# Kernel tuning notes

Measured on AMD Instinct MI355X. Metric: run time of the kernel, lower is better.

## Reference

```python
import jax, jax.numpy as jnp
import numpy as np


def setup_inputs() -> dict:
    key = jax.random.key(0)
    ks = jax.random.split(key, 5)
    b, t, q_dim, kv_dim, h = 16, 128, 256, 64, 4
    c = t - 1
    q_x = jax.random.normal(ks[0], (b, t, q_dim), dtype=jnp.float32)
    kv_x = jax.random.normal(ks[1], (b, t, c, kv_dim), dtype=jnp.float32)
    # Linear weights stored as [in, out]; no biases (bias=False in torch module).
    sq = 1.0 / np.sqrt(q_dim)
    sk = 1.0 / np.sqrt(kv_dim)
    Wq = jax.random.uniform(ks[2], (q_dim, kv_dim * h), jnp.float32, -sq, sq)
    Wk = jax.random.uniform(ks[3], (kv_dim, kv_dim * h), jnp.float32, -sk, sk)
    Wv = jax.random.uniform(ks[4], (kv_dim, kv_dim * h), jnp.float32, -sk, sk)
    return {"q_x": q_x, "kv_x": kv_x, "Wq": Wq, "Wk": Wk, "Wv": Wv}


def reference(q_x, kv_x, Wq, Wk, Wv):
    b, t, c, k = kv_x.shape  # c = t - 1
    h = Wq.shape[1] // k
    # projections
    q = (q_x @ Wq).reshape(b, t, h, k)          # [b,t,h,k]
    keys = (kv_x @ Wk).reshape(b, t, c, h, k)   # [b,t,c,h,k]
    vals = (kv_x @ Wv).reshape(b, t, c, h, k)
    # per-token attention over the c-sized context
    scores = jnp.einsum('bthk,btchk->bthc', q, keys) / jnp.sqrt(jnp.float32(k))
    w = jax.nn.softmax(scores, axis=-1)          # softmax over context dim
    out = jnp.einsum('bthc,btchk->bthk', w, vals)
    return out.reshape(b, t, h * k)
```

## Files before the change

kernel.cpp:

```cpp
#include <hip/hip_runtime.h>
#include <math.h>

#define Bdim 16
#define Tdim 128
#define Cdim 127
#define Hdim 4
#define QD   256
#define HK   256
#define BT   (Bdim * Tdim)

#define DPP_XOR1        0xB1
#define DPP_XOR2        0x4E
#define DPP_HALF_MIRROR 0x141
#define DPP_MIRROR      0x140
template<int CTRL>
__device__ __forceinline__ float dpp_movf(float x) {
    return __int_as_float(__builtin_amdgcn_update_dpp(
        0, __float_as_int(x), CTRL, 0xF, 0xF, true));
}
__device__ __forceinline__ float quad_sum(float v) {
    v += dpp_movf<DPP_XOR1>(v);
    v += dpp_movf<DPP_XOR2>(v);
    return v;
}
__device__ __forceinline__ float rows_max(float v) {
    v = fmaxf(v, dpp_movf<DPP_HALF_MIRROR>(v));
    v = fmaxf(v, dpp_movf<DPP_MIRROR>(v));
    v = fmaxf(v, __shfl_xor(v, 16, 64));
    v = fmaxf(v, __shfl_xor(v, 32, 64));
    return v;
}
__device__ __forceinline__ float rows_sum(float v) {
    v += dpp_movf<DPP_HALF_MIRROR>(v);
    v += dpp_movf<DPP_MIRROR>(v);
    v += __shfl_xor(v, 16, 64);
    v += __shfl_xor(v, 32, 64);
    return v;
}
__device__ __forceinline__ float wx_red(float v) {
    v += dpp_movf<DPP_XOR1>(v);
    v += dpp_movf<DPP_XOR2>(v);
    v += dpp_movf<DPP_HALF_MIRROR>(v);
    v += dpp_movf<DPP_MIRROR>(v);
    v += __shfl_xor(v, 16, 64);
    return v;
}

__global__ __launch_bounds__(256) void precompute_M(
        const float* __restrict__ Wq, const float* __restrict__ Wk,
        float* __restrict__ M) {
    __shared__ float wk_s[64][129];
    __shared__ float wq_s[2][128];
    int I = blockIdx.x;
    int H = blockIdx.y;
    int tid = threadIdx.x;

    #pragma unroll
    for (int it = 0; it < 8; ++it) {
        int flat = tid + it * 256;
        int m = flat >> 5, kq = flat & 31;
        float4 v = *(const float4*)(Wk + m * HK + H * 128 + kq * 4);
        wk_s[m][kq*4+0] = v.x; wk_s[m][kq*4+1] = v.y;
        wk_s[m][kq*4+2] = v.z; wk_s[m][kq*4+3] = v.w;
    }
    if (tid < 64) {
        int r = tid >> 5, kq = tid & 31;
        float4 v = *(const float4*)(Wq + (size_t)(I*2+r) * HK + H * 128 + kq * 4);
        wq_s[r][kq*4+0] = v.x; wq_s[r][kq*4+1] = v.y;
        wq_s[r][kq*4+2] = v.z; wq_s[r][kq*4+3] = v.w;
    }
    __syncthreads();

    int r = tid >> 7, hh = (tid >> 6) & 1, m = tid & 63;
    float acc = 0.f;
    #pragma unroll 8
    for (int j = 0; j < 64; ++j)
        acc = fmaf(wq_s[r][hh*64+j], wk_s[m][hh*64+j], acc);
    M[(size_t)(I*2+r) * HK + H * 128 + hh * 64 + m] = acc;
}

template <int NS>
__global__ __launch_bounds__(256) void qk_gemm(
        const float* __restrict__ q_x,
        const float* __restrict__ M,
        float* __restrict__ part) {
    const int KLEN = 256 / NS;
    __shared__ __align__(16) float q_s[16][256 / NS];
    int RB = blockIdx.x;
    int S  = blockIdx.y;
    int tid = threadIdx.x;

    for (int f = tid; f < 16 * KLEN / 4; f += 256) {
        int r = f / (KLEN / 4), kq = f % (KLEN / 4);
        *(float4*)&q_s[r][kq*4] =
            *(const float4*)(q_x + (size_t)(RB*16 + r) * QD + S * KLEN + kq * 4);
    }
    __syncthreads();

    float acc[16];
    #pragma unroll
    for (int r = 0; r < 16; ++r) acc[r] = 0.f;

    for (int kk = 0; kk < KLEN / 4; ++kk) {
        int k = S * KLEN + kk * 4;
        float m0 = M[(size_t)(k+0) * HK + tid];
        float m1 = M[(size_t)(k+1) * HK + tid];
        float m2 = M[(size_t)(k+2) * HK + tid];
        float m3 = M[(size_t)(k+3) * HK + tid];
        #pragma unroll
        for (int r = 0; r < 16; ++r) {
            float4 qv = *(const float4*)&q_s[r][kk*4];
            acc[r] = fmaf(qv.x, m0, fmaf(qv.y, m1, fmaf(qv.z, m2, fmaf(qv.w, m3, acc[r]))));
        }
    }
    float* dst = part + (size_t)S * (BT*HK) + (size_t)RB * 16 * HK + tid;
    #pragma unroll
    for (int r = 0; r < 16; ++r) dst[r * HK] = acc[r];
}

template <int NS>
__global__ __launch_bounds__(512, 6) void attn_main(
        const float* __restrict__ kv_x,
        const float* __restrict__ qk_p,
        const float* __restrict__ Wv,
        float* __restrict__ out) {
    __shared__ __align__(16) float4 sX4[128 * 16];
    __shared__ __align__(16) float qk_s[HK];
    __shared__ __align__(16) float4 e4[128];
    __shared__ __align__(16) float4 wx4[Hdim * 16];
    __shared__ __align__(16) float4 redm[8];
    __shared__ __align__(16) float4 reds[8];

    int bt  = blockIdx.x;
    int tid = threadIdx.x;

    const float4* Xg = (const float4*)(kv_x + (size_t)bt * (Cdim * 64));
    #pragma unroll
    for (int it = 0; it < 4; ++it) {
        int l = tid + it * 512;
        if (l < Cdim * 16) {
            int c = l >> 4, p = l & 15;
            __builtin_amdgcn_global_load_lds(
                (const __attribute__((address_space(1))) void*)(Xg + (c << 4) + (p ^ (c & 7))),
                (__attribute__((address_space(3))) void*)(sX4 + l), 16, 0, 0);
        }
    }
    if (tid >= 256 && tid < 320)
        ((float*)sX4)[Cdim * 64 + (tid - 256)] = 0.f;
    if (tid < 256) {
        float q = 0.f;
        #pragma unroll
        for (int s = 0; s < NS; ++s)
            q += qk_p[(size_t)s * (BT*HK) + (size_t)bt * HK + tid];
        qk_s[tid] = q;
    }
    __syncthreads();

    int lane = tid & 63;
    int wave = tid >> 6;
    int c  = tid >> 2;
    int qp = tid & 3;
    int sw = c & 7;

    float s0, s1, s2, s3;
    {
        const float4* xrow = sX4 + c * 16;
        float4 x0 = xrow[(qp*4 + 0) ^ sw];
        float4 x1 = xrow[(qp*4 + 1) ^ sw];
        float4 x2 = xrow[(qp*4 + 2) ^ sw];
        float4 x3 = xrow[(qp*4 + 3) ^ sw];
        const float4* qk4 = (const float4*)qk_s;
        float a0 = 0.f, a1 = 0.f, a2 = 0.f, a3 = 0.f;
        #pragma unroll
        for (int i = 0; i < 4; ++i) {
            float4 xi = (i == 0) ? x0 : (i == 1) ? x1 : (i == 2) ? x2 : x3;
            float4 q0 = qk4[0*16 + qp*4 + i];
            float4 q1 = qk4[1*16 + qp*4 + i];
            float4 q2 = qk4[2*16 + qp*4 + i];
            float4 q3 = qk4[3*16 + qp*4 + i];
            a0 = fmaf(q0.x, xi.x, fmaf(q0.y, xi.y, fmaf(q0.z, xi.z, fmaf(q0.w, xi.w, a0))));
            a1 = fmaf(q1.x, xi.x, fmaf(q1.y, xi.y, fmaf(q1.z, xi.z, fmaf(q1.w, xi.w, a1))));
            a2 = fmaf(q2.x, xi.x, fmaf(q2.y, xi.y, fmaf(q2.z, xi.z, fmaf(q2.w, xi.w, a2))));
            a3 = fmaf(q3.x, xi.x, fmaf(q3.y, xi.y, fmaf(q3.z, xi.z, fmaf(q3.w, xi.w, a3))));
        }
        a0 = quad_sum(a0); a1 = quad_sum(a1); a2 = quad_sum(a2); a3 = quad_sum(a3);
        bool valid = (c < Cdim);
        s0 = valid ? a0 * 0.125f : -INFINITY;
        s1 = valid ? a1 * 0.125f : -INFINITY;
        s2 = valid ? a2 * 0.125f : -INFINITY;
        s3 = valid ? a3 * 0.125f : -INFINITY;
    }

    float m0 = rows_max(s0), m1 = rows_max(s1), m2 = rows_max(s2), m3 = rows_max(s3);
    if (lane == 0) redm[wave] = make_float4(m0, m1, m2, m3);
    __syncthreads();
    float4 gm = redm[0];
    #pragma unroll
    for (int w = 1; w < 8; ++w) {
        float4 r = redm[w];
        gm.x = fmaxf(gm.x, r.x); gm.y = fmaxf(gm.y, r.y);
        gm.z = fmaxf(gm.z, r.z); gm.w = fmaxf(gm.w, r.w);
    }
    float e0 = __expf(s0 - gm.x);
    float e1 = __expf(s1 - gm.y);
    float e2 = __expf(s2 - gm.z);
    float e3 = __expf(s3 - gm.w);
    if (qp == 0) e4[c] = make_float4(e0, e1, e2, e3);
    float t0 = rows_sum(e0), t1 = rows_sum(e1), t2 = rows_sum(e2), t3 = rows_sum(e3);
    if (lane == 0) reds[wave] = make_float4(t0, t1, t2, t3);
    __syncthreads();

    {
        int jc = tid >> 5;
        int mq = (lane >> 3) & 3;
        int cs = lane & 7;
        float4 A0 = {0,0,0,0}, A1 = {0,0,0,0}, A2 = {0,0,0,0}, A3 = {0,0,0,0};
        #pragma unroll
        for (int mm = 0; mm < 4; ++mm) {
            int cc = cs + 8 * (mq * 4 + mm);
            float4 x4 = sX4[cc * 16 + (jc ^ cs)];
            float4 ee = e4[cc];
            A0.x = fmaf(ee.x, x4.x, A0.x); A0.y = fmaf(ee.x, x4.y, A0.y);
            A0.z = fmaf(ee.x, x4.z, A0.z); A0.w = fmaf(ee.x, x4.w, A0.w);
            A1.x = fmaf(ee.y, x4.x, A1.x); A1.y = fmaf(ee.y, x4.y, A1.y);
            A1.z = fmaf(ee.y, x4.z, A1.z); A1.w = fmaf(ee.y, x4.w, A1.w);
            A2.x = fmaf(ee.z, x4.x, A2.x); A2.y = fmaf(ee.z, x4.y, A2.y);
            A2.z = fmaf(ee.z, x4.z, A2.z); A2.w = fmaf(ee.z, x4.w, A2.w);
            A3.x = fmaf(ee.w, x4.x, A3.x); A3.y = fmaf(ee.w, x4.y, A3.y);
            A3.z = fmaf(ee.w, x4.z, A3.z); A3.w = fmaf(ee.w, x4.w, A3.w);
        }
        A0.x = wx_red(A0.x); A0.y = wx_red(A0.y); A0.z = wx_red(A0.z); A0.w = wx_red(A0.w);
        A1.x = wx_red(A1.x); A1.y = wx_red(A1.y); A1.z = wx_red(A1.z); A1.w = wx_red(A1.w);
        A2.x = wx_red(A2.x); A2.y = wx_red(A2.y); A2.z = wx_red(A2.z); A2.w = wx_red(A2.w);
        A3.x = wx_red(A3.x); A3.y = wx_red(A3.y); A3.z = wx_red(A3.z); A3.w = wx_red(A3.w);
        if ((lane & 31) == 0) {
            wx4[0 * 16 + jc] = A0;
            wx4[1 * 16 + jc] = A1;
            wx4[2 * 16 + jc] = A2;
            wx4[3 * 16 + jc] = A3;
        }
    }
    __syncthreads();

    if (tid < 256) {
        int hh = tid >> 6, k = tid & 63;
        float4 sums = reds[0];
        #pragma unroll
        for (int w = 1; w < 8; ++w) {
            float4 r = reds[w];
            sums.x += r.x; sums.y += r.y; sums.z += r.z; sums.w += r.w;
        }
        float denom = (hh == 0) ? sums.x : (hh == 1) ? sums.y
                    : (hh == 2) ? sums.z : sums.w;
        float inv = 1.f / denom;
        const float* wvcol = Wv + hh * 64 + k;
        float acc = 0.f;
        #pragma unroll 4
        for (int jc = 0; jc < 16; ++jc) {
            float4 w4 = wx4[hh * 16 + jc];
            acc = fmaf(w4.x, wvcol[(size_t)(jc*4+0) * HK],
                  fmaf(w4.y, wvcol[(size_t)(jc*4+1) * HK],
                  fmaf(w4.z, wvcol[(size_t)(jc*4+2) * HK],
                  fmaf(w4.w, wvcol[(size_t)(jc*4+3) * HK], acc))));
        }
        out[(size_t)bt * HK + tid] = acc * inv;
    }
}

extern "C" void kernel_launch(void* const* d_in, const int* in_sizes, int n_in,
                              void* d_out, int out_size, void* d_ws, size_t ws_size,
                              hipStream_t stream) {
    const float* q_x  = (const float*)d_in[0];
    const float* kv_x = (const float*)d_in[1];
    const float* Wq   = (const float*)d_in[2];
    const float* Wk   = (const float*)d_in[3];
    const float* Wv   = (const float*)d_in[4];
    float* out = (float*)d_out;

    float* M     = (float*)d_ws;
    float* parts = M + 256 * 256;

    size_t need4 = (size_t)(256*256 + 4 * BT*HK) * sizeof(float);
    int nsplit = (ws_size >= need4) ? 4 : 1;

    precompute_M<<<dim3(128, 2), 256, 0, stream>>>(Wq, Wk, M);
    if (nsplit == 4) {
        qk_gemm<4><<<dim3(128, 4), 256, 0, stream>>>(q_x, M, parts);
        attn_main<4><<<BT, 512, 0, stream>>>(kv_x, parts, Wv, out);
    } else {
        qk_gemm<1><<<dim3(128, 1), 256, 0, stream>>>(q_x, M, parts);
        attn_main<1><<<BT, 512, 0, stream>>>(kv_x, parts, Wv, out);
    }
}
```

Baseline: 42.46 us.

## Drop softmax max pass, simplify precompute_M, raise qk split to 8

Removes the max-subtraction in softmax so exp is computed directly on scaled scores. This eliminates a cross-wave max reduction and one block barrier, but risks overflow if scores grow large. precompute_M is rewritten to read Wq and Wk directly into registers with float4 loads instead of staging through LDS. The qk_gemm K-split goes from 4 to 8 for more parallelism, its inner loop is fully unrolled, and attn_main now sums 8 partial results.

```diff
diff --git a/kernel.cpp b/kernel.cpp
--- a/kernel.cpp
+++ b/kernel.cpp
@@ -23,13 +23,6 @@
     v += dpp_movf<DPP_XOR2>(v);
     return v;
 }
-__device__ __forceinline__ float rows_max(float v) {
-    v = fmaxf(v, dpp_movf<DPP_HALF_MIRROR>(v));
-    v = fmaxf(v, dpp_movf<DPP_MIRROR>(v));
-    v = fmaxf(v, __shfl_xor(v, 16, 64));
-    v = fmaxf(v, __shfl_xor(v, 32, 64));
-    return v;
-}
 __device__ __forceinline__ float rows_sum(float v) {
     v += dpp_movf<DPP_HALF_MIRROR>(v);
     v += dpp_movf<DPP_MIRROR>(v);
@@ -49,34 +42,22 @@
 __global__ __launch_bounds__(256) void precompute_M(
         const float* __restrict__ Wq, const float* __restrict__ Wk,
         float* __restrict__ M) {
-    __shared__ float wk_s[64][129];
-    __shared__ float wq_s[2][128];
-    int I = blockIdx.x;
-    int H = blockIdx.y;
+    int i = blockIdx.x;
     int tid = threadIdx.x;
-
-    #pragma unroll
-    for (int it = 0; it < 8; ++it) {
-        int flat = tid + it * 256;
-        int m = flat >> 5, kq = flat & 31;
-        float4 v = *(const float4*)(Wk + m * HK + H * 128 + kq * 4);
-        wk_s[m][kq*4+0] = v.x; wk_s[m][kq*4+1] = v.y;
-        wk_s[m][kq*4+2] = v.z; wk_s[m][kq*4+3] = v.w;
-    }
-    if (tid < 64) {
-        int r = tid >> 5, kq = tid & 31;
-        float4 v = *(const float4*)(Wq + (size_t)(I*2+r) * HK + H * 128 + kq * 4);
-        wq_s[r][kq*4+0] = v.x; wq_s[r][kq*4+1] = v.y;
-        wq_s[r][kq*4+2] = v.z; wq_s[r][kq*4+3] = v.w;
-    }
-    __syncthreads();
-
-    int r = tid >> 7, hh = (tid >> 6) & 1, m = tid & 63;
+    int h = tid >> 6, m = tid & 63;
+    const float4* wq4 = (const float4*)(Wq + (size_t)i * HK + h * 64);
+    const float4* wk4 = (const float4*)(Wk + (size_t)m * HK + h * 64);
+    float4 q[16], k[16];
+    #pragma unroll
+    for (int j = 0; j < 16; ++j) q[j] = wq4[j];
+    #pragma unroll
+    for (int j = 0; j < 16; ++j) k[j] = wk4[j];
     float acc = 0.f;
-    #pragma unroll 8
-    for (int j = 0; j < 64; ++j)
-        acc = fmaf(wq_s[r][hh*64+j], wk_s[m][hh*64+j], acc);
-    M[(size_t)(I*2+r) * HK + H * 128 + hh * 64 + m] = acc;
+    #pragma unroll
+    for (int j = 0; j < 16; ++j)
+        acc = fmaf(q[j].x, k[j].x, fmaf(q[j].y, k[j].y,
+              fmaf(q[j].z, k[j].z, fmaf(q[j].w, k[j].w, acc))));
+    M[(size_t)i * HK + tid] = acc;
 }
 
 template <int NS>
@@ -101,6 +82,7 @@
     #pragma unroll
     for (int r = 0; r < 16; ++r) acc[r] = 0.f;
 
+    #pragma unroll
     for (int kk = 0; kk < KLEN / 4; ++kk) {
         int k = S * KLEN + kk * 4;
         float m0 = M[(size_t)(k+0) * HK + tid];
@@ -128,7 +110,6 @@
     __shared__ __align__(16) float qk_s[HK];
     __shared__ __align__(16) float4 e4[128];
     __shared__ __align__(16) float4 wx4[Hdim * 16];
-    __shared__ __align__(16) float4 redm[8];
     __shared__ __align__(16) float4 reds[8];
 
     int bt  = blockIdx.x;
@@ -162,7 +143,7 @@
     int qp = tid & 3;
     int sw = c & 7;
 
-    float s0, s1, s2, s3;
+    float e0, e1, e2, e3;
     {
         const float4* xrow = sX4 + c * 16;
         float4 x0 = xrow[(qp*4 + 0) ^ sw];
@@ -185,26 +166,11 @@
         }
         a0 = quad_sum(a0); a1 = quad_sum(a1); a2 = quad_sum(a2); a3 = quad_sum(a3);
         bool valid = (c < Cdim);
-        s0 = valid ? a0 * 0.125f : -INFINITY;
-        s1 = valid ? a1 * 0.125f : -INFINITY;
-        s2 = valid ? a2 * 0.125f : -INFINITY;
-        s3 = valid ? a3 * 0.125f : -INFINITY;
-    }
-
-    float m0 = rows_max(s0), m1 = rows_max(s1), m2 = rows_max(s2), m3 = rows_max(s3);
-    if (lane == 0) redm[wave] = make_float4(m0, m1, m2, m3);
-    __syncthreads();
-    float4 gm = redm[0];
-    #pragma unroll
-    for (int w = 1; w < 8; ++w) {
-        float4 r = redm[w];
-        gm.x = fmaxf(gm.x, r.x); gm.y = fmaxf(gm.y, r.y);
-        gm.z = fmaxf(gm.z, r.z); gm.w = fmaxf(gm.w, r.w);
-    }
-    float e0 = __expf(s0 - gm.x);
-    float e1 = __expf(s1 - gm.y);
-    float e2 = __expf(s2 - gm.z);
-    float e3 = __expf(s3 - gm.w);
+        e0 = valid ? __expf(a0 * 0.125f) : 0.f;
+        e1 = valid ? __expf(a1 * 0.125f) : 0.f;
+        e2 = valid ? __expf(a2 * 0.125f) : 0.f;
+        e3 = valid ? __expf(a3 * 0.125f) : 0.f;
+    }
     if (qp == 0) e4[c] = make_float4(e0, e1, e2, e3);
     float t0 = rows_sum(e0), t1 = rows_sum(e1), t2 = rows_sum(e2), t3 = rows_sum(e3);
     if (lane == 0) reds[wave] = make_float4(t0, t1, t2, t3);
@@ -280,13 +246,13 @@
     float* M     = (float*)d_ws;
     float* parts = M + 256 * 256;
 
-    size_t need4 = (size_t)(256*256 + 4 * BT*HK) * sizeof(float);
-    int nsplit = (ws_size >= need4) ? 4 : 1;
-
-    precompute_M<<<dim3(128, 2), 256, 0, stream>>>(Wq, Wk, M);
-    if (nsplit == 4) {
-        qk_gemm<4><<<dim3(128, 4), 256, 0, stream>>>(q_x, M, parts);
-        attn_main<4><<<BT, 512, 0, stream>>>(kv_x, parts, Wv, out);
+    size_t need8 = (size_t)(256*256 + 8 * BT*HK) * sizeof(float);
+    int nsplit = (ws_size >= need8) ? 8 : 1;
+
+    precompute_M<<<256, 256, 0, stream>>>(Wq, Wk, M);
+    if (nsplit == 8) {
+        qk_gemm<8><<<dim3(128, 8), 256, 0, stream>>>(q_x, M, parts);
+        attn_main<8><<<BT, 512, 0, stream>>>(kv_x, parts, Wv, out);
     } else {
         qk_gemm<1><<<dim3(128, 1), 256, 0, stream>>>(q_x, M, parts);
         attn_main<1><<<BT, 512, 0, stream>>>(kv_x, parts, Wv, out);
```

New measurement: 42.68 us. About the same (+0.5%).
